# Performance work log

Measured on AMD Instinct MI355X. Metric: run time of the kernel, lower is better.

Reference implementation:

```python
import jax, jax.numpy as jnp
import numpy as np

ALPHA = 0.01  # ema_decay

def setup_inputs() -> dict:
    key = jax.random.key(0)
    k1, k2 = jax.random.split(key)
    B, S, H = 8, 2048, 2048
    x = jax.random.normal(k1, (B, S, H), dtype=jnp.float32)
    W = jax.random.normal(k2, (H, H), dtype=jnp.float32) * (1.0 / np.sqrt(H))
    b = jnp.zeros((H,), dtype=jnp.float32)
    return {"x": x, "W": W, "b": b}

def reference(x, W, b):
    B, S, H = x.shape
    dt = x.dtype
    # p = [S-1, S-2, ..., 0]; w_prime = (1-alpha)^p
    p = jnp.arange(S - 1, -1, -1, dtype=dt)
    one_m_a = jnp.asarray(1.0 - ALPHA, dtype=dt)
    w_prime = one_m_a ** p                                   # [S]
    # w = w_prime, but positions t>=1 scaled by alpha
    w = jnp.where(jnp.arange(S) >= 1, w_prime * ALPHA, w_prime)  # [S]
    c = jnp.cumsum(x * w[None, :, None], axis=1)             # [B,S,H]
    s = c / w_prime[None, :, None]                           # [B,S,H]
    # nn.Linear: s @ W^T + b
    return jnp.einsum('bsh,oh->bso', s, W) + b
```

## Files before the change

### kernel.cpp

```cpp
#include <hip/hip_runtime.h>
#include <cstdint>
#include <cstddef>

#define ALPHA 0.01f
#define A1    0.99f
#define B_    8
#define S_    2048
#define H_    2048
#define NCH   8
#define CL    256
#define NKT   32

typedef __attribute__((ext_vector_type(8))) short bf16x8;
typedef __attribute__((ext_vector_type(4))) float f32x4;

__device__ __forceinline__ unsigned short f2bf(float f) {
    unsigned int u = __float_as_uint(f);
    u += 0x7FFFu + ((u >> 16) & 1u);
    return (unsigned short)(u >> 16);
}

__device__ __forceinline__ void gld16(const void* g, void* l) {
    __builtin_amdgcn_global_load_lds(
        (const __attribute__((address_space(1))) unsigned int*)g,
        (__attribute__((address_space(3))) unsigned int*)l, 16, 0, 0);
}

__global__ void ema_cast_w(const float* __restrict__ W, short* __restrict__ Wb) {
    int i = (blockIdx.x * 256 + threadIdx.x) * 4;
    float4 v = *(const float4*)(W + i);
    short4 o;
    o.x = (short)f2bf(v.x);
    o.y = (short)f2bf(v.y);
    o.z = (short)f2bf(v.z);
    o.w = (short)f2bf(v.w);
    *(short4*)(Wb + i) = o;
}

__global__ void ema_carry_kernel(const float* __restrict__ x, float* __restrict__ carry) {
    int bid = blockIdx.x;
    int hg = bid & 7;
    int c  = (bid >> 3) & 7;
    int b  = bid >> 6;
    int h  = hg * 256 + threadIdx.x;
    const float* px = x + ((size_t)(b * S_) + c * CL) * H_ + h;
    float s;
    int i0;
    if (c == 0) { s = px[0]; i0 = 1; }
    else        { s = 0.f;   i0 = 0; }
    #pragma unroll 8
    for (int i = i0; i < CL; ++i)
        s = fmaf(A1, s, ALPHA * px[(size_t)i * H_]);
    carry[((b << 3) + c) * H_ + h] = s;
}

__global__ void ema_apply_kernel(const float* __restrict__ x, const float* __restrict__ carry,
                                 unsigned short* __restrict__ sb) {
    int bid = blockIdx.x;
    int hg = bid & 7;
    int c  = (bid >> 3) & 7;
    int b  = bid >> 6;
    int h  = hg * 256 + threadIdx.x;

    float A256 = A1;
    #pragma unroll
    for (int q = 0; q < 8; ++q) A256 *= A256;

    float ci = 0.f, f = 1.f;
    for (int j = c - 1; j >= 0; --j) {
        ci = fmaf(carry[((b << 3) + j) * H_ + h], f, ci);
        f *= A256;
    }

    size_t base = ((size_t)(b * S_) + c * CL) * H_ + h;
    const float* px = x + base;
    unsigned short* ps = sb + base;
    float s;
    int i0;
    if (c == 0) { s = px[0]; ps[0] = f2bf(s); i0 = 1; }
    else        { s = ci;    i0 = 0; }
    #pragma unroll 8
    for (int i = i0; i < CL; ++i) {
        s = fmaf(A1, s, ALPHA * px[(size_t)i * H_]);
        ps[(size_t)i * H_] = f2bf(s);
    }
}


#define BAR __builtin_amdgcn_s_barrier()
#define WAIT_LGKM do { asm volatile("s_waitcnt lgkmcnt(0)" ::: "memory"); \
                       __builtin_amdgcn_sched_barrier(0); } while (0)
#define VMW(n) asm volatile("s_waitcnt vmcnt(" #n ")" ::: "memory")

#define STGA(i, kt, buf) gld16(gA[i] + (size_t)(kt) * 128, &ldsA[buf][((i) << 12) + (w << 9)])
#define STGB(i, kt, buf) gld16(gB[i] + (size_t)(kt) * 128, &ldsB[buf][((i) << 12) + (w << 9)])

#define LDA(mh) do { int ra_ = (wm << 1) | (mh);                                   \
    const char* base_ = (const char*)&ldsA[cur][0]                                 \
        + (((((ra_ & 1) << 1) | (ra_ >> 1))) << 13) + laneRow;                     \
    _Pragma("unroll") for (int m_ = 0; m_ < 4; ++m_) {                             \
        Af[m_][0] = *(const bf16x8*)(base_ + (m_ << 11) + ck0);                    \
        Af[m_][1] = *(const bf16x8*)(base_ + (m_ << 11) + ck1); } } while (0)

#define LDB(nh) do { const char* base_ = (const char*)&ldsB[cur][0]                \
        + ((nh) << 14) + (wn << 12) + laneRow;                                     \
    _Pragma("unroll") for (int n_ = 0; n_ < 2; ++n_) {                             \
        Bf[(nh) * 2 + n_][0] = *(const bf16x8*)(base_ + (n_ << 11) + ck0);         \
        Bf[(nh) * 2 + n_][1] = *(const bf16x8*)(base_ + (n_ << 11) + ck1); } } while (0)

#define MM(mh, nh) do { __builtin_amdgcn_s_setprio(1);                             \
    _Pragma("unroll") for (int m_ = 0; m_ < 4; ++m_)                               \
    _Pragma("unroll") for (int n_ = 0; n_ < 2; ++n_)                               \
    _Pragma("unroll") for (int k_ = 0; k_ < 2; ++k_)                               \
        acc[(mh) * 4 + m_][(nh) * 2 + n_] = __builtin_amdgcn_mfma_f32_16x16x32_bf16( \
            Af[m_][k_], Bf[(nh) * 2 + n_][k_], acc[(mh) * 4 + m_][(nh) * 2 + n_], 0, 0, 0); \
    __builtin_amdgcn_s_setprio(0); } while (0)

__global__ __launch_bounds__(512, 2) void ema_gemm_kernel(
        const short* __restrict__ Sb, const short* __restrict__ Wb,
        const float* __restrict__ bias, float* __restrict__ out) {
    __shared__ short ldsA[2][16384];
    __shared__ short ldsB[2][16384];

    int bid = blockIdx.x;
    int swz = ((bid & 7) << 6) | (bid >> 3);
    int tm = swz >> 3;
    int tn = swz & 7;

    int tid  = threadIdx.x;
    int lane = tid & 63;
    int w    = tid >> 6;
    int wm   = w >> 2;
    int wn   = w & 3;

    const int K2 = H_ * 2;
    int rowA = tm << 8;
    int rowB = tn << 8;

    int rowoff = (w << 3) + (lane >> 3);
    int colb   = (((lane & 7) ^ (lane >> 3)) << 4);
    const char* SbB = (const char*)Sb;
    const char* WbB = (const char*)Wb;
    const char* gA[4];
    const char* gB[4];
    #pragma unroll
    for (int i = 0; i < 4; ++i) {
        int lq = ((i & 1) << 1) | (i >> 1);
        gA[i] = SbB + (size_t)(rowA + lq * 64 + rowoff) * K2 + colb;
        int pos = 2 * i + (w >> 2);
        int ls  = ((pos & 3) << 1) | (pos >> 2);
        gB[i] = WbB + (size_t)(rowB + ls * 32 + ((w & 3) << 3) + (lane >> 3)) * K2 + colb;
    }

    int laneRow = (lane & 15) << 7;
    int ck0 = (((lane >> 4)) ^ (lane & 7)) << 4;
    int ck1 = ((4 + (lane >> 4)) ^ (lane & 7)) << 4;

    f32x4 acc[8][4];
    #pragma unroll
    for (int i = 0; i < 8; ++i)
        #pragma unroll
        for (int j = 0; j < 4; ++j)
            acc[i][j] = (f32x4){0.f, 0.f, 0.f, 0.f};
    bf16x8 Af[4][2], Bf[4][2];

    int colg = (tn << 8) + (wn << 6) + (lane & 15);
    float bb[4];
    #pragma unroll
    for (int n = 0; n < 4; ++n) bb[n] = bias[colg + (n << 4)];

    STGA(0, 0, 0); STGA(1, 0, 0); STGB(0, 0, 0); STGB(1, 0, 0);
    STGA(2, 0, 0); STGA(3, 0, 0); STGB(2, 0, 0); STGB(3, 0, 0);
    STGA(0, 1, 1); STGA(1, 1, 1); STGB(0, 1, 1); STGB(1, 1, 1);
    VMW(6);
    BAR;

    for (int t = 0; t < NKT; ++t) {
        int cur = t & 1, nxt = cur ^ 1;
        bool i01 = (t < NKT - 1), i23 = (t < NKT - 2);
        LDA(0); LDB(0);
        if (i01) { STGA(2, t + 1, nxt); STGA(3, t + 1, nxt); }
        BAR; WAIT_LGKM;
        MM(0, 0);
        if (i01) { VMW(6); }
        BAR;
        LDB(1);
        if (i01) { STGB(2, t + 1, nxt); STGB(3, t + 1, nxt); }
        BAR; WAIT_LGKM;
        MM(0, 1);
        BAR;
        LDA(1);
        if (i23) { STGA(0, t + 2, cur); STGA(1, t + 2, cur); }
        BAR; WAIT_LGKM;
        MM(1, 0);
        BAR;
        if (i23) { STGB(0, t + 2, cur); STGB(1, t + 2, cur); }
        BAR;
        MM(1, 1);
        if (t == NKT - 2) { VMW(0); }
        else if (t < NKT - 2) { VMW(6); }
        BAR;
    }

    int rowg = (tm << 8) + (wm << 7) + ((lane >> 4) << 2);
    #pragma unroll
    for (int m = 0; m < 8; ++m) {
        #pragma unroll
        for (int n = 0; n < 4; ++n) {
            int c = colg + (n << 4);
            size_t rb = (size_t)(rowg + (m << 4)) << 11;
            #pragma unroll
            for (int q = 0; q < 4; ++q)
                out[rb + ((size_t)q << 11) + c] = acc[m][n][q] + bb[n];
        }
    }
}

extern "C" void kernel_launch(void* const* d_in, const int* in_sizes, int n_in,
                              void* d_out, int out_size, void* d_ws, size_t ws_size,
                              hipStream_t stream) {
    const float* x    = (const float*)d_in[0];
    const float* W    = (const float*)d_in[1];
    const float* bias = (const float*)d_in[2];
    float* out = (float*)d_out;

    char* ws = (char*)d_ws;
    size_t s_bytes = (size_t)B_ * S_ * H_ * 2;
    size_t w_bytes = (size_t)H_ * H_ * 2;
    unsigned short* s_bf = (unsigned short*)ws;
    short*          w_bf = (short*)(ws + s_bytes);
    float*          carry = (float*)(ws + s_bytes + w_bytes);

    ema_cast_w<<<(H_ * H_) / 1024, 256, 0, stream>>>(W, w_bf);
    ema_carry_kernel<<<B_ * NCH * (H_ / 256), 256, 0, stream>>>(x, carry);
    ema_apply_kernel<<<B_ * NCH * (H_ / 256), 256, 0, stream>>>(x, carry, s_bf);
    ema_gemm_kernel<<<(16384 / 256) * (2048 / 256), 512, 0, stream>>>(
        (const short*)s_bf, w_bf, bias, out);
}
```

Baseline: 211.9 us.

## Fuse EMA carry and apply into single-pass decoupled look-back scan; deepen GEMM prefetch

Replaces the separate carry and apply kernels with one scan kernel. Blocks are ordered chunk-major and chain their inclusive carries through global flags with acquire/release atomics, so each later chunk waits only on its predecessor. The chunk-0 blocks write the scan output in one pass, but blocks for chunks 1-6 still read x twice and only chunk 7 skips the local pass. The change also drops one kernel launch and the separate carry-combine loop, and it depends on blocks being scheduled in index order to avoid deadlock. The GEMM pipeline is reshuffled to prefetch a full K tile two steps ahead, with a changed waitcnt schedule.

```diff
diff --git a/kernel.cpp b/kernel.cpp
--- a/kernel.cpp
+++ b/kernel.cpp
@@ -26,7 +26,12 @@
         (__attribute__((address_space(3))) unsigned int*)l, 16, 0, 0);
 }
 
-__global__ void ema_cast_w(const float* __restrict__ W, short* __restrict__ Wb) {
+__global__ void ema_cast_w(const float* __restrict__ W, short* __restrict__ Wb,
+                           int* __restrict__ flags) {
+    if (blockIdx.x == 0) {
+        flags[threadIdx.x] = 0;
+        flags[threadIdx.x + 256] = 0;
+    }
     int i = (blockIdx.x * 256 + threadIdx.x) * 4;
     float4 v = *(const float4*)(W + i);
     short4 o;
@@ -37,50 +42,69 @@
     *(short4*)(Wb + i) = o;
 }
 
-__global__ void ema_carry_kernel(const float* __restrict__ x, float* __restrict__ carry) {
+__global__ __launch_bounds__(256) void ema_scan_kernel(
+        const float* __restrict__ x, unsigned short* __restrict__ sb,
+        float* __restrict__ carryInc, int* __restrict__ flags) {
     int bid = blockIdx.x;
+    int c  = bid >> 6;
+    int b  = (bid >> 3) & 7;
     int hg = bid & 7;
-    int c  = (bid >> 3) & 7;
-    int b  = bid >> 6;
-    int h  = hg * 256 + threadIdx.x;
-    const float* px = x + ((size_t)(b * S_) + c * CL) * H_ + h;
-    float s;
-    int i0;
-    if (c == 0) { s = px[0]; i0 = 1; }
-    else        { s = 0.f;   i0 = 0; }
-    #pragma unroll 8
-    for (int i = i0; i < CL; ++i)
-        s = fmaf(A1, s, ALPHA * px[(size_t)i * H_]);
-    carry[((b << 3) + c) * H_ + h] = s;
-}
-
-__global__ void ema_apply_kernel(const float* __restrict__ x, const float* __restrict__ carry,
-                                 unsigned short* __restrict__ sb) {
-    int bid = blockIdx.x;
-    int hg = bid & 7;
-    int c  = (bid >> 3) & 7;
-    int b  = bid >> 6;
-    int h  = hg * 256 + threadIdx.x;
-
-    float A256 = A1;
-    #pragma unroll
-    for (int q = 0; q < 8; ++q) A256 *= A256;
-
-    float ci = 0.f, f = 1.f;
-    for (int j = c - 1; j >= 0; --j) {
-        ci = fmaf(carry[((b << 3) + j) * H_ + h], f, ci);
-        f *= A256;
-    }
-
-    size_t base = ((size_t)(b * S_) + c * CL) * H_ + h;
+    int h  = (hg << 8) + threadIdx.x;
+    size_t base = ((size_t)(b * S_) + (size_t)c * CL) * H_ + h;
     const float* px = x + base;
     unsigned short* ps = sb + base;
-    float s;
-    int i0;
-    if (c == 0) { s = px[0]; ps[0] = f2bf(s); i0 = 1; }
-    else        { s = ci;    i0 = 0; }
+
+    float A256 = A1;
+    #pragma unroll
+    for (int q = 0; q < 8; ++q) A256 *= A256;
+
+    if (c == 0) {
+        float s = px[0];
+        ps[0] = f2bf(s);
+        #pragma unroll 8
+        for (int i = 1; i < CL; ++i) {
+            s = fmaf(A1, s, ALPHA * px[(size_t)i * H_]);
+            ps[(size_t)i * H_] = f2bf(s);
+        }
+        carryInc[((b << 3) + 0) * H_ + h] = s;
+        __threadfence();
+        __syncthreads();
+        if (threadIdx.x == 0)
+            __hip_atomic_store(&flags[((b << 3) << 3) | hg], 1,
+                               __ATOMIC_RELEASE, __HIP_MEMORY_SCOPE_AGENT);
+        return;
+    }
+
+    float loc = 0.f;
+    if (c < 7) {
+        #pragma unroll 8
+        for (int i = 0; i < CL; ++i)
+            loc = fmaf(A1, loc, ALPHA * px[(size_t)i * H_]);
+    }
+
+    int pf = (((b << 3) + (c - 1)) << 3) | hg;
+    if (threadIdx.x == 0) {
+        while (__hip_atomic_load(&flags[pf], __ATOMIC_ACQUIRE,
+                                 __HIP_MEMORY_SCOPE_AGENT) == 0)
+            __builtin_amdgcn_s_sleep(4);
+    }
+    __syncthreads();
+    float prev = __hip_atomic_load(&carryInc[((b << 3) + (c - 1)) * H_ + h],
+                                   __ATOMIC_RELAXED, __HIP_MEMORY_SCOPE_AGENT);
+
+    if (c < 7) {
+        float inc = fmaf(A256, prev, loc);
+        carryInc[((b << 3) + c) * H_ + h] = inc;
+        __threadfence();
+        __syncthreads();
+        if (threadIdx.x == 0)
+            __hip_atomic_store(&flags[(((b << 3) + c) << 3) | hg], 1,
+                               __ATOMIC_RELEASE, __HIP_MEMORY_SCOPE_AGENT);
+    }
+
+    float s = prev;
     #pragma unroll 8
-    for (int i = i0; i < CL; ++i) {
+    for (int i = 0; i < CL; ++i) {
         s = fmaf(A1, s, ALPHA * px[(size_t)i * H_]);
         ps[(size_t)i * H_] = f2bf(s);
     }
@@ -172,33 +196,34 @@
     STGA(0, 0, 0); STGA(1, 0, 0); STGB(0, 0, 0); STGB(1, 0, 0);
     STGA(2, 0, 0); STGA(3, 0, 0); STGB(2, 0, 0); STGB(3, 0, 0);
     STGA(0, 1, 1); STGA(1, 1, 1); STGB(0, 1, 1); STGB(1, 1, 1);
-    VMW(6);
+    STGA(2, 1, 1); STGA(3, 1, 1); STGB(2, 1, 1); STGB(3, 1, 1);
+    VMW(8);
     BAR;
 
     for (int t = 0; t < NKT; ++t) {
-        int cur = t & 1, nxt = cur ^ 1;
-        bool i01 = (t < NKT - 1), i23 = (t < NKT - 2);
+        int cur = t & 1;
+        bool stg = (t < NKT - 2);
         LDA(0); LDB(0);
-        if (i01) { STGA(2, t + 1, nxt); STGA(3, t + 1, nxt); }
+        asm volatile("s_waitcnt lgkmcnt(8)" ::: "memory");
         BAR; WAIT_LGKM;
         MM(0, 0);
-        if (i01) { VMW(6); }
         BAR;
         LDB(1);
-        if (i01) { STGB(2, t + 1, nxt); STGB(3, t + 1, nxt); }
+        if (stg) { STGA(0, t + 2, cur); STGA(1, t + 2, cur);
+                   STGB(0, t + 2, cur); STGB(1, t + 2, cur); }
         BAR; WAIT_LGKM;
         MM(0, 1);
         BAR;
         LDA(1);
-        if (i23) { STGA(0, t + 2, cur); STGA(1, t + 2, cur); }
+        if (stg) { STGB(2, t + 2, cur); STGB(3, t + 2, cur); }
         BAR; WAIT_LGKM;
         MM(1, 0);
         BAR;
-        if (i23) { STGB(0, t + 2, cur); STGB(1, t + 2, cur); }
+        if (stg) { STGA(2, t + 2, cur); STGA(3, t + 2, cur); }
         BAR;
         MM(1, 1);
-        if (t == NKT - 2) { VMW(0); }
-        else if (t < NKT - 2) { VMW(6); }
+        if (t < NKT - 2)       { VMW(8); }
+        else if (t == NKT - 2) { VMW(0); }
         BAR;
     }
 
@@ -227,13 +252,14 @@
     char* ws = (char*)d_ws;
     size_t s_bytes = (size_t)B_ * S_ * H_ * 2;
     size_t w_bytes = (size_t)H_ * H_ * 2;
-    unsigned short* s_bf = (unsigned short*)ws;
-    short*          w_bf = (short*)(ws + s_bytes);
+    size_t c_bytes = (size_t)B_ * NCH * H_ * 4;
+    unsigned short* s_bf  = (unsigned short*)ws;
+    short*          w_bf  = (short*)(ws + s_bytes);
     float*          carry = (float*)(ws + s_bytes + w_bytes);
-
-    ema_cast_w<<<(H_ * H_) / 1024, 256, 0, stream>>>(W, w_bf);
-    ema_carry_kernel<<<B_ * NCH * (H_ / 256), 256, 0, stream>>>(x, carry);
-    ema_apply_kernel<<<B_ * NCH * (H_ / 256), 256, 0, stream>>>(x, carry, s_bf);
+    int*            flags = (int*)(ws + s_bytes + w_bytes + c_bytes);
+
+    ema_cast_w<<<(H_ * H_) / 1024, 256, 0, stream>>>(W, w_bf, flags);
+    ema_scan_kernel<<<B_ * NCH * (H_ / 256), 256, 0, stream>>>(x, s_bf, carry, flags);
     ema_gemm_kernel<<<(16384 / 256) * (2048 / 256), 512, 0, stream>>>(
         (const short*)s_bf, w_bf, bias, out);
 }
```

Result: slower. 504.1 us (+137.9%).
